# Kernel optimization log

Hardware: AMD Instinct MI355X
Metric: run time of the kernel (lower is better)

Reference implementation:

```python
import jax, jax.numpy as jnp
import numpy as np

C, H, W = 512, 192, 192  # feature map dims; 3x3 patches at stride 3 (non-overlapping)


def setup_inputs() -> dict:
    key = jax.random.key(0)
    k1, k2 = jax.random.split(key)
    model_resp = jax.random.normal(k1, (1, C, H, W), dtype=jnp.float32)
    style_resp = jax.random.normal(k2, (1, C, H, W), dtype=jnp.float32)
    return {"model_resp": model_resp, "style_resp": style_resp}


def _unfold3(x):
    # torch.nn.Unfold(kernel=3, stride=3) on (1, C, H, W) -> (C*9, L) after the
    # module's view(patch_count, patch_size) (note: rows are feature channels,
    # columns are spatial locations, matching the original code's dim order).
    _, c, h, w = x.shape
    p = x[0].reshape(c, h // 3, 3, w // 3, 3)          # (c, ph, kh, pw, kw)
    p = p.transpose(0, 2, 4, 1, 3)                      # (c, kh, kw, ph, pw)
    return p.reshape(c * 9, (h // 3) * (w // 3))        # (A, L)


def reference(model_resp, style_resp):
    img = _unfold3(model_resp)                          # (A, L)
    sty = _unfold3(style_resp)                          # (A, L)
    img_norm = 1.0 / jnp.linalg.norm(img, axis=1)       # (A,)
    sty_norm = 1.0 / jnp.linalg.norm(sty, axis=1)       # (A,)
    S = img @ sty.T                                     # (A, A), S[i,j] = img_i . sty_j
    # Faithful to torch: expand(A, A) of a 1-D tensor broadcasts along dim 0,
    # i.e. multiplies COLUMNS by the normalizer vector.
    S1 = S * img_norm[None, :]
    S2 = S1.T * sty_norm[None, :]                       # S2[i,j] = img_norm[i]*sty_norm[j]*(img_j . sty_i)
    nearest = jnp.argmax(S2, axis=0)                    # (A,) int
    max_sim = jnp.max(S2, axis=0)                       # (A,) float (the online-max values)
    return nearest, max_sim
```

## Files before the change

### kernel.cpp

```cpp
#include <hip/hip_runtime.h>
#include <hip/hip_bf16.h>
#include <hip/hip_fp16.h>

#define A_DIM 4608
#define L_DIM 4096
#define CH    512
#define H_DIM 192
#define W_DIM 192

#define BM 128
#define BN 128
#define BK 32
#define NS (L_DIM / BK)

typedef _Float16 half8 __attribute__((ext_vector_type(8)));
typedef float   floatx4 __attribute__((ext_vector_type(4)));
typedef float   floatx16 __attribute__((ext_vector_type(16)));

__global__ __launch_bounds__(256) void prep_kernel(
    const float* __restrict__ x0, const float* __restrict__ x1,
    _Float16* __restrict__ Uhi0, _Float16* __restrict__ Ulo0,
    _Float16* __restrict__ Uhi1, _Float16* __restrict__ Ulo1,
    float* __restrict__ nr0, float* __restrict__ nr1) {
  const int which = blockIdx.z;
  const float* __restrict__ x = which ? x1 : x0;
  _Float16* __restrict__ Uhi = which ? Uhi1 : Uhi0;
  _Float16* __restrict__ Ulo = which ? Ulo1 : Ulo0;
  float* __restrict__ nrecip = which ? nr1 : nr0;

  const int c = blockIdx.x, kh = blockIdx.y;
  const int a0 = c * 9 + kh * 3;
  const float* __restrict__ xb = x + (size_t)c * (H_DIM * W_DIM) + kh * W_DIM;
  const int t = threadIdx.x;

  float ss0 = 0.f, ss1 = 0.f, ss2 = 0.f;
#pragma unroll
  for (int it = 0; it < 16; ++it) {
    const int l = it * 256 + t;
    const int ph = l >> 6, pw = l & 63;
    const float* __restrict__ p = xb + (3 * ph) * W_DIM + 3 * pw;
    const float v0 = p[0], v1 = p[1], v2 = p[2];
    ss0 += v0 * v0; ss1 += v1 * v1; ss2 += v2 * v2;
    const _Float16 h0 = (_Float16)v0, h1 = (_Float16)v1, h2 = (_Float16)v2;
    const size_t base = ((size_t)(l >> 3) * A_DIM) * 8 + (l & 7);
    Uhi[base + (size_t)(a0 + 0) * 8] = h0;
    Uhi[base + (size_t)(a0 + 1) * 8] = h1;
    Uhi[base + (size_t)(a0 + 2) * 8] = h2;
    Ulo[base + (size_t)(a0 + 0) * 8] = (_Float16)(v0 - (float)h0);
    Ulo[base + (size_t)(a0 + 1) * 8] = (_Float16)(v1 - (float)h1);
    Ulo[base + (size_t)(a0 + 2) * 8] = (_Float16)(v2 - (float)h2);
  }
  __shared__ float wss[3][4];
  const int wid = t >> 6, lane = t & 63;
  float s[3] = {ss0, ss1, ss2};
#pragma unroll
  for (int kw = 0; kw < 3; ++kw) {
    float v = s[kw];
#pragma unroll
    for (int off = 32; off > 0; off >>= 1) v += __shfl_down(v, off, 64);
    if (lane == 0) wss[kw][wid] = v;
  }
  __syncthreads();
  if (t < 3) {
    const float tot = wss[t][0] + wss[t][1] + wss[t][2] + wss[t][3];
    nrecip[a0 + t] = 1.0f / sqrtf(tot);
  }
}

#define GLDS(g, l)                                                          \
  __builtin_amdgcn_global_load_lds(                                        \
      (const __attribute__((address_space(1))) void*)(g),                   \
      (__attribute__((address_space(3))) void*)(l), 16, 0, 0)

__global__ __launch_bounds__(256, 2) void gemm_max_kernel(
    const _Float16* __restrict__ Shi, const _Float16* __restrict__ Slo,
    const _Float16* __restrict__ Ihi, const _Float16* __restrict__ Ilo,
    const float* __restrict__ img_nr,
    unsigned long long* __restrict__ packed) {
  __shared__ _Float16 sm[2][4][4 * 128 * 8];

  const int t = threadIdx.x;
  const int lane = t & 63, wv = t >> 6;
  const int wvr = wv >> 1, wvc = wv & 1;
  const int row0 = blockIdx.y * BM;
  const int col0 = blockIdx.x * BN;
  const int l31 = lane & 31, hs = lane >> 5;

  floatx16 acc[2][2];
#pragma unroll
  for (int rf = 0; rf < 2; ++rf)
#pragma unroll
    for (int cf = 0; cf < 2; ++cf) acc[rf][cf] = (floatx16)0.f;

  const size_t CH8 = (size_t)A_DIM * 8;
  const size_t so = (size_t)(t & 127) * 8 + (size_t)(t >> 7) * CH8;
  const _Float16* __restrict__ pAh = Shi + (size_t)row0 * 8 + so;
  const _Float16* __restrict__ pAl = Slo + (size_t)row0 * 8 + so;
  const _Float16* __restrict__ pBh = Ihi + (size_t)col0 * 8 + so;
  const _Float16* __restrict__ pBl = Ilo + (size_t)col0 * 8 + so;
  const int dl = t * 8;

#define ISSUE(b, off)                                      \
  do {                                                     \
    GLDS(pAh + (off),           &sm[b][0][dl]);            \
    GLDS(pAh + (off) + 2 * CH8, &sm[b][0][dl + 2048]);     \
    GLDS(pAl + (off),           &sm[b][1][dl]);            \
    GLDS(pAl + (off) + 2 * CH8, &sm[b][1][dl + 2048]);     \
    GLDS(pBh + (off),           &sm[b][2][dl]);            \
    GLDS(pBh + (off) + 2 * CH8, &sm[b][2][dl + 2048]);     \
    GLDS(pBl + (off),           &sm[b][3][dl]);            \
    GLDS(pBl + (off) + 2 * CH8, &sm[b][3][dl + 2048]);     \
  } while (0)

  ISSUE(0, 0);

  for (int ks = 0; ks < NS; ++ks) {
    const int cur = ks & 1;
    if (ks + 1 < NS) {
      ISSUE(1 - cur, (size_t)(ks + 1) * 4 * CH8);
      asm volatile("s_waitcnt vmcnt(8)" ::: "memory");
    } else {
      asm volatile("s_waitcnt vmcnt(0)" ::: "memory");
    }
    asm volatile("s_barrier" ::: "memory");

#pragma unroll
    for (int kk = 0; kk < 2; ++kk) {
      const int kc = kk * 2 + hs;
      half8 ah[2], al[2], bh[2], bl[2];
#pragma unroll
      for (int rf = 0; rf < 2; ++rf) {
        const int idx = (kc * 128 + wvr * 64 + rf * 32 + l31) * 8;
        ah[rf] = *(const half8*)&sm[cur][0][idx];
        al[rf] = *(const half8*)&sm[cur][1][idx];
      }
#pragma unroll
      for (int cf = 0; cf < 2; ++cf) {
        const int idx = (kc * 128 + wvc * 64 + cf * 32 + l31) * 8;
        bh[cf] = *(const half8*)&sm[cur][2][idx];
        bl[cf] = *(const half8*)&sm[cur][3][idx];
      }
#pragma unroll
      for (int rf = 0; rf < 2; ++rf)
#pragma unroll
        for (int cf = 0; cf < 2; ++cf)
          acc[rf][cf] = __builtin_amdgcn_mfma_f32_32x32x16_f16(
              ah[rf], bh[cf], acc[rf][cf], 0, 0, 0);
#pragma unroll
      for (int rf = 0; rf < 2; ++rf)
#pragma unroll
        for (int cf = 0; cf < 2; ++cf)
          acc[rf][cf] = __builtin_amdgcn_mfma_f32_32x32x16_f16(
              ah[rf], bl[cf], acc[rf][cf], 0, 0, 0);
#pragma unroll
      for (int rf = 0; rf < 2; ++rf)
#pragma unroll
        for (int cf = 0; cf < 2; ++cf)
          acc[rf][cf] = __builtin_amdgcn_mfma_f32_32x32x16_f16(
              al[rf], bh[cf], acc[rf][cf], 0, 0, 0);
    }
    asm volatile("s_barrier" ::: "memory");
  }

#pragma unroll
  for (int cf = 0; cf < 2; ++cf) {
    const int j = col0 + wvc * 64 + cf * 32 + l31;
    float best = -3.4e38f;
    int bi = 0x7FFFFFFF;
#pragma unroll
    for (int rf = 0; rf < 2; ++rf) {
      const int base_i = row0 + wvr * 64 + rf * 32 + 4 * hs;
#pragma unroll
      for (int g = 0; g < 4; ++g) {
        const floatx4 n4 = *(const floatx4*)&img_nr[base_i + 8 * g];
#pragma unroll
        for (int r = 0; r < 4; ++r) {
          const int i = base_i + 8 * g + r;
          const float v = acc[rf][cf][g * 4 + r] * n4[r];
          if (v > best) { best = v; bi = i; }
        }
      }
    }
    const float ov = __shfl_xor(best, 32, 64);
    const int oi = __shfl_xor(bi, 32, 64);
    if (ov > best || (ov == best && oi < bi)) { best = ov; bi = oi; }
    if (hs == 0) {
      const unsigned u = __float_as_uint(best);
      const unsigned key = (u & 0x80000000u) ? ~u : (u | 0x80000000u);
      const unsigned long long pk =
          ((unsigned long long)key << 32) | (unsigned)(~(unsigned)bi);
      atomicMax(&packed[j], pk);
    }
  }
}

__global__ __launch_bounds__(256) void finalize_kernel(
    const unsigned long long* __restrict__ packed,
    const float* __restrict__ sty_nr, float* __restrict__ out) {
  const int j = blockIdx.x * 256 + threadIdx.x;
  if (j >= A_DIM) return;
  const unsigned long long p = packed[j];
  const unsigned key = (unsigned)(p >> 32);
  const unsigned u = (key & 0x80000000u) ? (key ^ 0x80000000u) : ~key;
  const float v = __uint_as_float(u);
  const int idx = (int)(~(unsigned)(p & 0xFFFFFFFFu));
  out[j] = (float)idx;
  out[A_DIM + j] = v * sty_nr[j];
}

extern "C" void kernel_launch(void* const* d_in, const int* in_sizes, int n_in,
                              void* d_out, int out_size, void* d_ws, size_t ws_size,
                              hipStream_t stream) {
  const float* model = (const float*)d_in[0];
  const float* style = (const float*)d_in[1];
  float* out = (float*)d_out;
  char* ws = (char*)d_ws;

  const size_t usz = (size_t)A_DIM * L_DIM * 2;
  _Float16* img_hi = (_Float16*)(ws);
  _Float16* img_lo = (_Float16*)(ws + usz);
  _Float16* sty_hi = (_Float16*)(ws + 2 * usz);
  _Float16* sty_lo = (_Float16*)(ws + 3 * usz);
  float* img_nr = (float*)(ws + 4 * usz);
  float* sty_nr = img_nr + A_DIM;
  unsigned long long* packed = (unsigned long long*)(img_nr + 2 * A_DIM);

  hipMemsetAsync(packed, 0, (size_t)A_DIM * 8, stream);
  prep_kernel<<<dim3(CH, 3, 2), 256, 0, stream>>>(
      model, style, img_hi, img_lo, sty_hi, sty_lo, img_nr, sty_nr);
  gemm_max_kernel<<<dim3(A_DIM / BN, A_DIM / BM), 256, 0, stream>>>(
      sty_hi, sty_lo, img_hi, img_lo, img_nr, packed);
  finalize_kernel<<<18, 256, 0, stream>>>(packed, sty_nr, out);
}
```

Before: 798.2 us.

## Restage prep through LDS for coalesced stores and restructure GEMM pipeline barriers

The prep kernel now handles 32 channels for one patch row per block. It reads rows with vector loads, transposes the hi/lo fp16 split through swizzled shared memory and writes 16-byte coalesced stores, replacing scattered 2-byte stores. Squared norms are accumulated with atomics into a zeroed buffer, and the reciprocal square root moves into the GEMM epilogue and the finalize kernel. The GEMM loop now waits for all loads, barriers once, then issues the next prefetch, which removes the second barrier per iteration but makes load overlap shallower.

```diff
diff --git a/kernel.cpp b/kernel.cpp
--- a/kernel.cpp
+++ b/kernel.cpp
@@ -13,6 +13,8 @@
 #define BK 32
 #define NS (L_DIM / BK)
 
+#define CPB 32
+
 typedef _Float16 half8 __attribute__((ext_vector_type(8)));
 typedef float   floatx4 __attribute__((ext_vector_type(4)));
 typedef float   floatx16 __attribute__((ext_vector_type(16)));
@@ -21,50 +23,73 @@
     const float* __restrict__ x0, const float* __restrict__ x1,
     _Float16* __restrict__ Uhi0, _Float16* __restrict__ Ulo0,
     _Float16* __restrict__ Uhi1, _Float16* __restrict__ Ulo1,
-    float* __restrict__ nr0, float* __restrict__ nr1) {
+    float* __restrict__ ss0, float* __restrict__ ss1) {
   const int which = blockIdx.z;
   const float* __restrict__ x = which ? x1 : x0;
   _Float16* __restrict__ Uhi = which ? Uhi1 : Uhi0;
   _Float16* __restrict__ Ulo = which ? Ulo1 : Ulo0;
-  float* __restrict__ nrecip = which ? nr1 : nr0;
-
-  const int c = blockIdx.x, kh = blockIdx.y;
-  const int a0 = c * 9 + kh * 3;
-  const float* __restrict__ xb = x + (size_t)c * (H_DIM * W_DIM) + kh * W_DIM;
+  float* __restrict__ ssg = which ? ss1 : ss0;
+
+  const int ph = blockIdx.y;
+  const int c0 = blockIdx.x * CPB;
+  const int abase = blockIdx.x * (CPB * 9);
+
+  __shared__ _Float16 sHi[CPB * 9 * 8 * 8];
+  __shared__ _Float16 sLo[CPB * 9 * 8 * 8];
+  __shared__ float ssb[CPB * 9];
+
   const int t = threadIdx.x;
-
-  float ss0 = 0.f, ss1 = 0.f, ss2 = 0.f;
-#pragma unroll
-  for (int it = 0; it < 16; ++it) {
-    const int l = it * 256 + t;
-    const int ph = l >> 6, pw = l & 63;
-    const float* __restrict__ p = xb + (3 * ph) * W_DIM + 3 * pw;
-    const float v0 = p[0], v1 = p[1], v2 = p[2];
-    ss0 += v0 * v0; ss1 += v1 * v1; ss2 += v2 * v2;
-    const _Float16 h0 = (_Float16)v0, h1 = (_Float16)v1, h2 = (_Float16)v2;
-    const size_t base = ((size_t)(l >> 3) * A_DIM) * 8 + (l & 7);
-    Uhi[base + (size_t)(a0 + 0) * 8] = h0;
-    Uhi[base + (size_t)(a0 + 1) * 8] = h1;
-    Uhi[base + (size_t)(a0 + 2) * 8] = h2;
-    Ulo[base + (size_t)(a0 + 0) * 8] = (_Float16)(v0 - (float)h0);
-    Ulo[base + (size_t)(a0 + 1) * 8] = (_Float16)(v1 - (float)h1);
-    Ulo[base + (size_t)(a0 + 2) * 8] = (_Float16)(v2 - (float)h2);
-  }
-  __shared__ float wss[3][4];
-  const int wid = t >> 6, lane = t & 63;
-  float s[3] = {ss0, ss1, ss2};
-#pragma unroll
-  for (int kw = 0; kw < 3; ++kw) {
-    float v = s[kw];
-#pragma unroll
-    for (int off = 32; off > 0; off >>= 1) v += __shfl_down(v, off, 64);
-    if (lane == 0) wss[kw][wid] = v;
-  }
+  for (int a = t; a < CPB * 9; a += 256) ssb[a] = 0.f;
   __syncthreads();
-  if (t < 3) {
-    const float tot = wss[t][0] + wss[t][1] + wss[t][2] + wss[t][3];
-    nrecip[a0 + t] = 1.0f / sqrtf(tot);
-  }
+
+  const int c_l = t >> 3;
+  const int s = t & 7;
+  const float* __restrict__ rowbase =
+      x + ((size_t)(c0 + c_l) * H_DIM + 3 * ph) * W_DIM + s * 24;
+  float ssp[9] = {0.f, 0.f, 0.f, 0.f, 0.f, 0.f, 0.f, 0.f, 0.f};
+
+#pragma unroll
+  for (int kh = 0; kh < 3; ++kh) {
+    const float* __restrict__ rp = rowbase + kh * W_DIM;
+    floatx4 v4[6];
+#pragma unroll
+    for (int i = 0; i < 6; ++i) v4[i] = *(const floatx4*)(rp + i * 4);
+    half8 hv[3], lv[3];
+#pragma unroll
+    for (int i = 0; i < 6; ++i)
+#pragma unroll
+      for (int j = 0; j < 4; ++j) {
+        const int m = i * 4 + j;
+        const int kw = m % 3, e = m / 3;
+        const float v = v4[i][j];
+        ssp[kh * 3 + kw] += v * v;
+        const _Float16 h = (_Float16)v;
+        hv[kw][e] = h;
+        lv[kw][e] = (_Float16)(v - (float)h);
+      }
+#pragma unroll
+    for (int kw = 0; kw < 3; ++kw) {
+      const int a_l = c_l * 9 + kh * 3 + kw;
+      const int addr = (a_l * 8 + (s ^ (a_l & 7))) * 8;
+      *(half8*)&sHi[addr] = hv[kw];
+      *(half8*)&sLo[addr] = lv[kw];
+    }
+  }
+#pragma unroll
+  for (int q = 0; q < 9; ++q) atomicAdd(&ssb[c_l * 9 + q], ssp[q]);
+  __syncthreads();
+
+#pragma unroll
+  for (int i = 0; i < 9; ++i) {
+    const int idx = i * 256 + t;
+    const int c8 = idx / 288;
+    const int a_l = idx - c8 * 288;
+    const int addr = (a_l * 8 + (c8 ^ (a_l & 7))) * 8;
+    const size_t g = ((size_t)(ph * 8 + c8) * A_DIM + abase + a_l) * 8;
+    *(half8*)&Uhi[g] = *(const half8*)&sHi[addr];
+    *(half8*)&Ulo[g] = *(const half8*)&sLo[addr];
+  }
+  for (int a = t; a < CPB * 9; a += 256) atomicAdd(&ssg[abase + a], ssb[a]);
 }
 
 #define GLDS(g, l)                                                          \
@@ -75,7 +100,7 @@
 __global__ __launch_bounds__(256, 2) void gemm_max_kernel(
     const _Float16* __restrict__ Shi, const _Float16* __restrict__ Slo,
     const _Float16* __restrict__ Ihi, const _Float16* __restrict__ Ilo,
-    const float* __restrict__ img_nr,
+    const float* __restrict__ img_ss,
     unsigned long long* __restrict__ packed) {
   __shared__ _Float16 sm[2][4][4 * 128 * 8];
 
@@ -116,13 +141,9 @@
 
   for (int ks = 0; ks < NS; ++ks) {
     const int cur = ks & 1;
-    if (ks + 1 < NS) {
-      ISSUE(1 - cur, (size_t)(ks + 1) * 4 * CH8);
-      asm volatile("s_waitcnt vmcnt(8)" ::: "memory");
-    } else {
-      asm volatile("s_waitcnt vmcnt(0)" ::: "memory");
-    }
+    asm volatile("s_waitcnt vmcnt(0)" ::: "memory");
     asm volatile("s_barrier" ::: "memory");
+    if (ks + 1 < NS) ISSUE(1 - cur, (size_t)(ks + 1) * 4 * CH8);
 
 #pragma unroll
     for (int kk = 0; kk < 2; ++kk) {
@@ -159,9 +180,19 @@
           acc[rf][cf] = __builtin_amdgcn_mfma_f32_32x32x16_f16(
               al[rf], bh[cf], acc[rf][cf], 0, 0, 0);
     }
-    asm volatile("s_barrier" ::: "memory");
-  }
-
+  }
+
+  float nrv[2][16];
+#pragma unroll
+  for (int rf = 0; rf < 2; ++rf) {
+    const int base_i = row0 + wvr * 64 + rf * 32 + 4 * hs;
+#pragma unroll
+    for (int g = 0; g < 4; ++g) {
+      const floatx4 s4 = *(const floatx4*)&img_ss[base_i + 8 * g];
+#pragma unroll
+      for (int r = 0; r < 4; ++r) nrv[rf][g * 4 + r] = 1.0f / sqrtf(s4[r]);
+    }
+  }
 #pragma unroll
   for (int cf = 0; cf < 2; ++cf) {
     const int j = col0 + wvc * 64 + cf * 32 + l31;
@@ -171,15 +202,13 @@
     for (int rf = 0; rf < 2; ++rf) {
       const int base_i = row0 + wvr * 64 + rf * 32 + 4 * hs;
 #pragma unroll
-      for (int g = 0; g < 4; ++g) {
-        const floatx4 n4 = *(const floatx4*)&img_nr[base_i + 8 * g];
+      for (int g = 0; g < 4; ++g)
 #pragma unroll
         for (int r = 0; r < 4; ++r) {
           const int i = base_i + 8 * g + r;
-          const float v = acc[rf][cf][g * 4 + r] * n4[r];
+          const float v = acc[rf][cf][g * 4 + r] * nrv[rf][g * 4 + r];
           if (v > best) { best = v; bi = i; }
         }
-      }
     }
     const float ov = __shfl_xor(best, 32, 64);
     const int oi = __shfl_xor(bi, 32, 64);
@@ -196,7 +225,7 @@
 
 __global__ __launch_bounds__(256) void finalize_kernel(
     const unsigned long long* __restrict__ packed,
-    const float* __restrict__ sty_nr, float* __restrict__ out) {
+    const float* __restrict__ sty_ss, float* __restrict__ out) {
   const int j = blockIdx.x * 256 + threadIdx.x;
   if (j >= A_DIM) return;
   const unsigned long long p = packed[j];
@@ -205,7 +234,7 @@
   const float v = __uint_as_float(u);
   const int idx = (int)(~(unsigned)(p & 0xFFFFFFFFu));
   out[j] = (float)idx;
-  out[A_DIM + j] = v * sty_nr[j];
+  out[A_DIM + j] = v * (1.0f / sqrtf(sty_ss[j]));
 }
 
 extern "C" void kernel_launch(void* const* d_in, const int* in_sizes, int n_in,
@@ -221,14 +250,14 @@
   _Float16* img_lo = (_Float16*)(ws + usz);
   _Float16* sty_hi = (_Float16*)(ws + 2 * usz);
   _Float16* sty_lo = (_Float16*)(ws + 3 * usz);
-  float* img_nr = (float*)(ws + 4 * usz);
-  float* sty_nr = img_nr + A_DIM;
-  unsigned long long* packed = (unsigned long long*)(img_nr + 2 * A_DIM);
-
-  hipMemsetAsync(packed, 0, (size_t)A_DIM * 8, stream);
-  prep_kernel<<<dim3(CH, 3, 2), 256, 0, stream>>>(
-      model, style, img_hi, img_lo, sty_hi, sty_lo, img_nr, sty_nr);
+  float* img_ss = (float*)(ws + 4 * usz);
+  float* sty_ss = img_ss + A_DIM;
+  unsigned long long* packed = (unsigned long long*)(img_ss + 2 * A_DIM);
+
+  hipMemsetAsync(img_ss, 0, (size_t)A_DIM * 16, stream);
+  prep_kernel<<<dim3(CH / CPB, H_DIM / 3, 2), 256, 0, stream>>>(
+      model, style, img_hi, img_lo, sty_hi, sty_lo, img_ss, sty_ss);
   gemm_max_kernel<<<dim3(A_DIM / BN, A_DIM / BM), 256, 0, stream>>>(
-      sty_hi, sty_lo, img_hi, img_lo, img_nr, packed);
-  finalize_kernel<<<18, 256, 0, stream>>>(packed, sty_nr, out);
-}
+      sty_hi, sty_lo, img_hi, img_lo, img_ss, packed);
+  finalize_kernel<<<18, 256, 0, stream>>>(packed, sty_ss, out);
+}
```

After: 743.9 us. 1.07x faster.
